# Kernel optimization log

Hardware: AMD Instinct MI355X
Metric: run time of the kernel (lower is better)

Reference implementation:

```python
import jax, jax.numpy as jnp
import numpy as np

NUM_HEADS = 16
THETA = 10000.0


def _apply_rope(x, pos):
    # x: [b, h, t, d_k], pos: [t] int
    d = x.shape[-1]
    inv_freq = THETA ** (-jnp.arange(0, d, 2, dtype=jnp.float32) / d)  # [d/2]
    ang = pos.astype(jnp.float32)[:, None] * inv_freq                  # [t, d/2]
    cos, sin = jnp.cos(ang), jnp.sin(ang)
    x1, x2 = x[..., ::2], x[..., 1::2]
    r1 = x1 * cos - x2 * sin
    r2 = x1 * sin + x2 * cos
    return jnp.stack([r1, r2], axis=-1).reshape(x.shape)


def setup_inputs() -> dict:
    key = jax.random.key(0)
    k1, k2, k3 = jax.random.split(key, 3)
    b, t, dm = 4, 2048, 2048
    in_features = jax.random.normal(k1, (b, t, dm), dtype=jnp.float32)
    token_positions = jnp.arange(t, dtype=jnp.int64)
    W_qkv = jax.random.normal(k2, (3 * dm, dm), dtype=jnp.float32) * 0.02
    W_o = jax.random.normal(k3, (dm, dm), dtype=jnp.float32) * 0.02
    return {"in_features": in_features, "token_positions": token_positions,
            "W_qkv": W_qkv, "W_o": W_o}


def reference(in_features, token_positions, W_qkv, W_o):
    b, t, dm = in_features.shape
    h = NUM_HEADS
    dk = dm // h
    # fused QKV projection (Linear: y = x W^T)
    qkv = in_features @ W_qkv.T                       # [b, t, 3*dm]
    q, k, v = jnp.split(qkv, 3, axis=-1)
    def to_heads(x):
        return x.reshape(b, t, h, dk).transpose(0, 2, 1, 3)  # [b, h, t, dk]
    q, k, v = to_heads(q), to_heads(k), to_heads(v)
    q = _apply_rope(q, token_positions)
    k = _apply_rope(k, token_positions)
    # causal SDPA
    scale = 1.0 / np.sqrt(dk).astype(np.float32)
    scores = jnp.einsum('bhqd,bhkd->bhqk', q, k) * scale
    causal = jnp.tril(jnp.ones((t, t), dtype=bool))
    scores = jnp.where(causal, scores, jnp.finfo(scores.dtype).min)
    attn = jax.nn.softmax(scores, axis=-1)
    out = jnp.einsum('bhqk,bhkd->bhqd', attn, v)      # [b, h, t, dk]
    out = out.transpose(0, 2, 1, 3).reshape(b, t, dm)
    return out @ W_o.T
```

## Files before the change

kernel.cpp:

```cpp
#include <hip/hip_runtime.h>

typedef unsigned short u16;
typedef __attribute__((ext_vector_type(8))) short s8v;
typedef __attribute__((ext_vector_type(8))) __bf16 bf8;
typedef __attribute__((ext_vector_type(4))) float f4v;

#define GLB(p) ((const __attribute__((address_space(1))) void*)(p))
#define LDS(p) ((__attribute__((address_space(3))) void*)(p))

static __device__ __forceinline__ float b2f(u16 u) {
    union { unsigned int i; float f; } v; v.i = ((unsigned int)u) << 16; return v.f;
}
static __device__ __forceinline__ u16 f2b(float f) {
    union { float f; unsigned int i; } v; v.f = f;
    v.i += 0x7fffu + ((v.i >> 16) & 1u);
    return (u16)(v.i >> 16);
}

__global__ __launch_bounds__(256) void k_conv(const float* __restrict__ X,
                                              const float* __restrict__ Wq,
                                              const float* __restrict__ Wo,
                                              u16* __restrict__ Xb,
                                              u16* __restrict__ Wqb,
                                              u16* __restrict__ Wob) {
    int i = blockIdx.x * 256 + threadIdx.x;
    const float* in; u16* out; int off;
    if (i < 4194304)      { in = X;  out = Xb;  off = i; }
    else if (i < 7340032) { in = Wq; out = Wqb; off = i - 4194304; }
    else                  { in = Wo; out = Wob; off = i - 7340032; }
    float4 v = ((const float4*)in)[off];
    union { u16 u[4]; unsigned long long ll; } o;
    o.u[0] = f2b(v.x); o.u[1] = f2b(v.y); o.u[2] = f2b(v.z); o.u[3] = f2b(v.w);
    ((unsigned long long*)out)[off] = o.ll;
}

template<int MODE>
__global__ __launch_bounds__(512, 2) void k_gemm_bt(
    const u16* __restrict__ A, const u16* __restrict__ B,
    int K, int N, int gx,
    u16* __restrict__ Qb, u16* __restrict__ Kb, u16* __restrict__ Vt,
    float* __restrict__ Cf, const int* __restrict__ pos)
{
    extern __shared__ __align__(16) u16 Ls[];

    const int t    = threadIdx.x;
    const int lane = t & 63;
    const int wid  = t >> 6;
    const int wm = wid >> 2, wn = wid & 3;
    const int la = lane & 15, lb = lane >> 4;

    const int bid = (int)blockIdx.x;
    const int id2 = (bid & 7) * ((int)gridDim.x >> 3) + (bid >> 3);
    const int bx = id2 % gx, by = id2 / gx;
    const long arow0 = (long)by * 256;
    const long brow0 = (long)bx * 256;

    const int sr = t >> 2;
    const int sg = (t & 3) ^ (sr & 3);
    const u16* Asrc = A + (arow0 + sr) * (long)K + sg * 8;
    const u16* Bsrc = B + (brow0 + sr) * (long)K + sg * 8;
    const long K128 = 128 * (long)K;
    u16* ldst = Ls + t * 8;

#define STG(q_, kt_) do {                                                          \
        const long ko_ = (long)(kt_) * 32;                                         \
        u16* d_ = ldst + (q_) * 16384;                                             \
        __builtin_amdgcn_global_load_lds(GLB(Asrc + ko_),         LDS(d_),         16, 0, 0); \
        __builtin_amdgcn_global_load_lds(GLB(Asrc + K128 + ko_),  LDS(d_ + 4096),  16, 0, 0); \
        __builtin_amdgcn_global_load_lds(GLB(Bsrc + ko_),         LDS(d_ + 8192),  16, 0, 0); \
        __builtin_amdgcn_global_load_lds(GLB(Bsrc + K128 + ko_),  LDS(d_ + 12288), 16, 0, 0); \
    } while (0)
#define RD(off) (*(const bf8*)(Ls + (off)))

    f4v acc[8][4];
#pragma unroll
    for (int m = 0; m < 8; m++)
#pragma unroll
        for (int n = 0; n < 4; n++) acc[m][n] = (f4v){0.f, 0.f, 0.f, 0.f};

    const int gA = (lb ^ (la & 3)) * 8;
    const int aBase = wm * 4096 + la * 32 + gA;
    const int bBase = 8192 + (wn >> 1) * 4096 + ((wn & 1) * 64 + la) * 32 + gA;

    const int NKT = K >> 5;
    STG(0, 0); STG(1, 1);
    asm volatile("s_waitcnt vmcnt(4)" ::: "memory");
    __builtin_amdgcn_s_barrier();

    for (int X = 0; X < NKT; ++X) {
        const int D = (X % 3) * 16384;
        int S = X + 2; if (S > NKT - 1) S = NKT - 1;
        STG((X + 2) % 3, S);

        bf8 aF[8], bF[4];
#pragma unroll
        for (int mi = 0; mi < 8; mi++) aF[mi] = RD(D + aBase + mi * 512);
#pragma unroll
        for (int ni = 0; ni < 4; ni++) bF[ni] = RD(D + bBase + ni * 512);

        __builtin_amdgcn_s_setprio(1);
#pragma unroll
        for (int mi = 0; mi < 8; mi++)
#pragma unroll
            for (int ni = 0; ni < 4; ni++)
                acc[mi][ni] = __builtin_amdgcn_mfma_f32_16x16x32_bf16(aF[mi], bF[ni], acc[mi][ni], 0, 0, 0);
        __builtin_amdgcn_s_setprio(0);

        asm volatile("s_waitcnt vmcnt(4)" ::: "memory");
        __builtin_amdgcn_s_barrier();
    }
    asm volatile("s_waitcnt vmcnt(0)" ::: "memory");
#undef STG
#undef RD

    if (MODE == 1) {
#pragma unroll
        for (int mi = 0; mi < 8; mi++)
#pragma unroll
            for (int ni = 0; ni < 4; ni++) {
                const long grow0 = arow0 + wm * 128 + mi * 16 + lb * 4;
                const int  gcol  = (int)brow0 + wn * 64 + ni * 16 + la;
#pragma unroll
                for (int i = 0; i < 4; i++)
                    Cf[(grow0 + i) * (long)N + gcol] = acc[mi][ni][i];
            }
        return;
    }

    __syncthreads();
    const int part = (int)(brow0 >> 11);
    const int colp = (int)brow0 & 2047;
    const int h0   = colp >> 7;
    const int bidx = (int)(arow0 >> 11);
    const int t0   = (int)arow0 & 2047;

    if (part == 2) {
#pragma unroll
        for (int mi = 0; mi < 8; mi++)
#pragma unroll
            for (int ni = 0; ni < 4; ni++) {
                const int tlb = wm * 128 + mi * 16 + lb * 4;
                const int dl  = wn * 64 + ni * 16 + la;
#pragma unroll
                for (int i2 = 0; i2 < 2; i2++) {
                    unsigned int pk = (unsigned int)f2b(acc[mi][ni][i2 * 2])
                                    | ((unsigned int)f2b(acc[mi][ni][i2 * 2 + 1]) << 16);
                    *(unsigned int*)(Ls + dl * 264 + tlb + i2 * 2) = pk;
                }
            }
        __syncthreads();
#pragma unroll
        for (int j = 0; j < 16; j++) {
            const int dl = j * 16 + wid * 2 + (lane >> 5);
            const int c  = lane & 31;
            bf8 v = *(const bf8*)(Ls + dl * 264 + c * 8);
            const long bh = (long)(bidx * 16 + h0 + (dl >> 7));
            *(bf8*)(Vt + (bh << 18) + ((long)(dl & 127) << 11) + t0 + c * 8) = v;
        }
    } else {
        u16* dst = (part == 0) ? Qb : Kb;
#pragma unroll
        for (int mi = 0; mi < 8; mi++)
#pragma unroll
            for (int ni = 0; ni < 4; ni++) {
                const int tlb = wm * 128 + mi * 16 + lb * 4;
                const int dl  = wn * 64 + ni * 16 + la;
#pragma unroll
                for (int i = 0; i < 4; i++)
                    Ls[(tlb + i) * 264 + dl] = f2b(acc[mi][ni][i]);
            }
        __syncthreads();
        const int c = t & 15;
        float invf[4];
#pragma unroll
        for (int p2 = 0; p2 < 4; p2++)
            invf[p2] = exp2f((float)(c * 4 + p2) * -0.20762050593046014f);
#pragma unroll
        for (int j = 0; j < 16; j++) {
            const int R  = j * 32 + (t >> 4);
            const int tl = R >> 1, hh = R & 1;
            s8v v = *(const s8v*)(Ls + tl * 264 + hh * 128 + c * 8);
            const float pf = (float)pos[t0 + tl];
            union { u16 u[8]; s8v v; } ov;
#pragma unroll
            for (int p2 = 0; p2 < 4; p2++) {
                float x1 = b2f((u16)v[2 * p2]);
                float x2 = b2f((u16)v[2 * p2 + 1]);
                float sn, cs;
                __sincosf(pf * invf[p2], &sn, &cs);
                ov.u[2 * p2]     = f2b(x1 * cs - x2 * sn);
                ov.u[2 * p2 + 1] = f2b(x1 * sn + x2 * cs);
            }
            const long bh = (long)(bidx * 16 + h0 + hh);
            *(s8v*)(dst + ((bh << 11) + t0 + tl) * 128 + c * 8) = ov.v;
        }
    }
}

__global__ __launch_bounds__(512) void k_attn(const u16* __restrict__ Qb,
                                              const u16* __restrict__ Kb,
                                              const u16* __restrict__ Vt,
                                              u16* __restrict__ Ob)
{
    __shared__ __align__(16) u16 Ks[2][32 * 128];
    __shared__ __align__(16) u16 Vs[2][64 * 64];
    __shared__ __align__(16) u16 Pl[8][32 * 32];

    const int tid  = threadIdx.x;
    const int lane = tid & 63;
    const int w    = tid >> 6;
    const int la = lane & 15, lb = lane >> 4;
    const int qg = 7 - ((int)blockIdx.x >> 6);
    const int bh = blockIdx.x & 63;
    const long base = (long)bh << 18;
    const int qt = qg * 8 + w;
    const int q0 = qt * 32;
    const int tiles_w = qt + 1;
    const int NT = qg * 8 + 8;
    const float scale = 0.08838834764831845f;

    bf8 qf[2][4];
#pragma unroll
    for (int m = 0; m < 2; m++)
#pragma unroll
        for (int kb = 0; kb < 4; kb++)
            qf[m][kb] = *(const bf8*)(Qb + base + (long)(q0 + m * 16 + la) * 128 + kb * 32 + lb * 8);

    f4v o[2][8];
#pragma unroll
    for (int m = 0; m < 2; m++)
#pragma unroll
        for (int n = 0; n < 8; n++) o[m][n] = (f4v){0.f, 0.f, 0.f, 0.f};
    float lst[2][4];
#pragma unroll
    for (int m = 0; m < 2; m++)
#pragma unroll
        for (int i = 0; i < 4; i++) lst[m][i] = 0.f;

    char* Pb = (char*)(Pl[w]);

    const int ko = tid * 16;
    const int kr = ko >> 8, kc = (ko & 255) ^ ((kr & 7) << 4);
    const int vo = tid * 16;
    const int vR = vo >> 7, vc = (vo & 127) ^ ((vR & 7) << 4);
    const int vd = 2 * vR + (vc >> 6), vt = (vc & 63) >> 1;

#define STAGE(buf, jt_) do {                                                        \
        const int kv0_ = (jt_) * 32;                                               \
        __builtin_amdgcn_global_load_lds(                                          \
            GLB(Kb + base + (long)(kv0_ + kr) * 128 + (kc >> 1)),                  \
            LDS((u16*)Ks[buf] + tid * 8), 16, 0, 0);                               \
        __builtin_amdgcn_global_load_lds(                                          \
            GLB(Vt + base + ((long)vd << 11) + kv0_ + vt),                         \
            LDS((u16*)Vs[buf] + tid * 8), 16, 0, 0);                               \
    } while (0)

    STAGE(0, 0);

    for (int jt = 0; jt < NT; ++jt) {
        const int buf = jt & 1;
        __syncthreads();
        if (jt + 1 < NT) STAGE(buf ^ 1, jt + 1);

        if (jt < tiles_w) {
            const char* KsB = (const char*)Ks[buf];
            const char* VsB = (const char*)Vs[buf];

            f4v s[2][2];
            s[0][0] = s[0][1] = s[1][0] = s[1][1] = (f4v){0.f, 0.f, 0.f, 0.f};
#pragma unroll
            for (int n = 0; n < 2; n++) {
                const int row = n * 16 + la;
#pragma unroll
                for (int kb = 0; kb < 4; kb++) {
                    bf8 kf = *(const bf8*)(KsB + row * 256 + ((kb * 64 + lb * 16) ^ ((row & 7) << 4)));
                    s[0][n] = __builtin_amdgcn_mfma_f32_16x16x32_bf16(qf[0][kb], kf, s[0][n], 0, 0, 0);
                    s[1][n] = __builtin_amdgcn_mfma_f32_16x16x32_bf16(qf[1][kb], kf, s[1][n], 0, 0, 0);
                }
            }

            bf8 vf[8];
#pragma unroll
            for (int nO = 0; nO < 8; nO++) {
                const int R = nO * 8 + (la >> 1);
                vf[nO] = *(const bf8*)(VsB + R * 128 + (((la & 1) * 64 + lb * 16) ^ ((R & 7) << 4)));
            }

            const bool diag = (jt == qt);
            float p[2][2][4];
#pragma unroll
            for (int m = 0; m < 2; m++)
#pragma unroll
                for (int n = 0; n < 2; n++)
#pragma unroll
                    for (int i = 0; i < 4; i++) {
                        float v = __expf(fmaf(s[m][n][i], scale, -8.0f));
                        if (diag && (n * 16 + la) > (m * 16 + lb * 4 + i)) v = 0.f;
                        p[m][n][i] = v;
                        lst[m][i] += v;
                    }

#pragma unroll
            for (int m = 0; m < 2; m++)
#pragma unroll
                for (int n = 0; n < 2; n++)
#pragma unroll
                    for (int i = 0; i < 4; i++) {
                        const int row = m * 16 + lb * 4 + i;
                        const int colb = (n * 16 + la) * 2;
                        *(u16*)(Pb + row * 64 + (colb ^ ((row & 3) << 4))) = f2b(p[m][n][i]);
                    }
            bf8 pa[2];
#pragma unroll
            for (int am = 0; am < 2; am++) {
                const int row = am * 16 + la;
                pa[am] = *(const bf8*)(Pb + row * 64 + ((lb * 16) ^ ((row & 3) << 4)));
            }
#pragma unroll
            for (int nO = 0; nO < 8; nO++) {
                o[0][nO] = __builtin_amdgcn_mfma_f32_16x16x32_bf16(pa[0], vf[nO], o[0][nO], 0, 0, 0);
                o[1][nO] = __builtin_amdgcn_mfma_f32_16x16x32_bf16(pa[1], vf[nO], o[1][nO], 0, 0, 0);
            }
        }
        __syncthreads();
    }
#undef STAGE

    float linv[2][4];
#pragma unroll
    for (int m = 0; m < 2; m++)
#pragma unroll
        for (int i = 0; i < 4; i++) {
            float l = lst[m][i];
            l += __shfl_xor(l, 1);
            l += __shfl_xor(l, 2);
            l += __shfl_xor(l, 4);
            l += __shfl_xor(l, 8);
            linv[m][i] = 1.0f / l;
        }

    const int b = bh >> 4, h = bh & 15;
#pragma unroll
    for (int m = 0; m < 2; m++)
#pragma unroll
        for (int nO = 0; nO < 8; nO++)
#pragma unroll
            for (int i = 0; i < 4; i++) {
                const int row = q0 + m * 16 + lb * 4 + i;
                const int d = nO * 16 + la;
                Ob[((long)(b * 2048 + row) << 11) + h * 128 + d] = f2b(o[m][nO][i] * linv[m][i]);
            }
}

extern "C" void kernel_launch(void* const* d_in, const int* in_sizes, int n_in,
                              void* d_out, int out_size, void* d_ws, size_t ws_size,
                              hipStream_t stream)
{
    const float* X    = (const float*)d_in[0];
    const int*   pos  = (const int*)d_in[1];
    const float* Wqkv = (const float*)d_in[2];
    const float* Wo   = (const float*)d_in[3];
    float* out = (float*)d_out;

    char* ws = (char*)d_ws;
    u16* Xb    = (u16*)(ws + 0);
    u16* Wqkvb = (u16*)(ws + 33554432);
    u16* Wob   = (u16*)(ws + 58720256);
    u16* Qb    = (u16*)(ws + 67108864);
    u16* Kb    = (u16*)(ws + 100663296);
    u16* Vt    = (u16*)(ws + 134217728);
    u16* Ob    = (u16*)(ws + 167772160);

    k_conv<<<32768, 256, 0, stream>>>(X, Wqkv, Wo, Xb, Wqkvb, Wob);
    k_gemm_bt<0><<<768, 512, 135168, stream>>>(Xb, Wqkvb, 2048, 6144, 24, Qb, Kb, Vt, nullptr, pos);
    k_attn<<<512, 512, 0, stream>>>(Qb, Kb, Vt, Ob);
    k_gemm_bt<1><<<256, 512, 98304, stream>>>(Ob, Wob, 2048, 2048, 8, nullptr, nullptr, nullptr, out, nullptr);
}
```

Baseline: 455.0 us.

## Shrink GEMM LDS footprint with double buffering and half-tile epilogue; narrow output GEMM tile

The GEMM switches from a triple-buffered LDS pipeline to double buffering with a new 8-way XOR swizzled layout. The QKV epilogue now stages one 128-row half of the tile at a time, so shared memory per block drops by half. The output projection uses 256x128 tiles and twice as many blocks, giving better CU coverage on the 2048x2048 result. The aim is higher occupancy and better load balance, at the cost of shallower prefetch and a full vmcnt(0) wait plus barrier every k-step.

Result: faster. 423.0 us (-7.0%).

```diff
diff --git a/kernel.cpp b/kernel.cpp
--- a/kernel.cpp
+++ b/kernel.cpp
@@ -41,6 +41,9 @@
     u16* __restrict__ Qb, u16* __restrict__ Kb, u16* __restrict__ Vt,
     float* __restrict__ Cf, const int* __restrict__ pos)
 {
+    constexpr int BN   = MODE ? 128 : 256;
+    constexpr int NB   = MODE ? 2 : 4;
+    constexpr int BUFS = MODE ? 12288 : 16384;
     extern __shared__ __align__(16) u16 Ls[];
 
     const int t    = threadIdx.x;
@@ -53,63 +56,79 @@
     const int id2 = (bid & 7) * ((int)gridDim.x >> 3) + (bid >> 3);
     const int bx = id2 % gx, by = id2 / gx;
     const long arow0 = (long)by * 256;
-    const long brow0 = (long)bx * 256;
-
-    const int sr = t >> 2;
-    const int sg = (t & 3) ^ (sr & 3);
-    const u16* Asrc = A + (arow0 + sr) * (long)K + sg * 8;
-    const u16* Bsrc = B + (brow0 + sr) * (long)K + sg * 8;
-    const long K128 = 128 * (long)K;
-    u16* ldst = Ls + t * 8;
-
-#define STG(q_, kt_) do {                                                          \
-        const long ko_ = (long)(kt_) * 32;                                         \
-        u16* d_ = ldst + (q_) * 16384;                                             \
-        __builtin_amdgcn_global_load_lds(GLB(Asrc + ko_),         LDS(d_),         16, 0, 0); \
-        __builtin_amdgcn_global_load_lds(GLB(Asrc + K128 + ko_),  LDS(d_ + 4096),  16, 0, 0); \
-        __builtin_amdgcn_global_load_lds(GLB(Bsrc + ko_),         LDS(d_ + 8192),  16, 0, 0); \
-        __builtin_amdgcn_global_load_lds(GLB(Bsrc + K128 + ko_),  LDS(d_ + 12288), 16, 0, 0); \
+    const long brow0 = (long)bx * BN;
+
+    const int r0 = t >> 3, sl = t & 7;
+    const int sA0 = sl ^ (r0 & 7);
+    const int sA1 = sl ^ ((r0 + 64) & 7);
+    const long RA0 = r0 + 128 * (sA0 >> 2);
+    const long RA1 = 64 + r0 + 128 * (sA1 >> 2);
+    const u16* As0 = A + (arow0 + RA0) * (long)K + (sA0 & 3) * 8;
+    const u16* As1 = A + (arow0 + RA1) * (long)K + (sA1 & 3) * 8;
+    const u16 *Bsrc0, *Bsrc1;
+    if (MODE == 0) {
+        Bsrc0 = B + (brow0 + RA0) * (long)K + (sA0 & 3) * 8;
+        Bsrc1 = B + (brow0 + RA1) * (long)K + (sA1 & 3) * 8;
+    } else {
+        const long RB0 = r0 + 64 * (sA0 >> 2);
+        Bsrc0 = B + (brow0 + RB0) * (long)K + (sA0 & 3) * 8;
+        Bsrc1 = nullptr;
+    }
+
+#define STG(q_, kt_) do {                                                        \
+        const long ko_ = (long)(kt_) * 32;                                       \
+        u16* d_ = Ls + (q_) * BUFS + t * 8;                                      \
+        __builtin_amdgcn_global_load_lds(GLB(As0 + ko_),   LDS(d_),         16, 0, 0); \
+        __builtin_amdgcn_global_load_lds(GLB(As1 + ko_),   LDS(d_ + 4096),  16, 0, 0); \
+        __builtin_amdgcn_global_load_lds(GLB(Bsrc0 + ko_), LDS(d_ + 8192),  16, 0, 0); \
+        if (MODE == 0)                                                           \
+            __builtin_amdgcn_global_load_lds(GLB(Bsrc1 + ko_), LDS(d_ + 12288), 16, 0, 0); \
     } while (0)
 #define RD(off) (*(const bf8*)(Ls + (off)))
 
-    f4v acc[8][4];
+    f4v acc[8][NB];
 #pragma unroll
     for (int m = 0; m < 8; m++)
 #pragma unroll
-        for (int n = 0; n < 4; n++) acc[m][n] = (f4v){0.f, 0.f, 0.f, 0.f};
-
-    const int gA = (lb ^ (la & 3)) * 8;
-    const int aBase = wm * 4096 + la * 32 + gA;
-    const int bBase = 8192 + (wn >> 1) * 4096 + ((wn & 1) * 64 + la) * 32 + gA;
+        for (int n = 0; n < NB; n++) acc[m][n] = (f4v){0.f, 0.f, 0.f, 0.f};
+
+    const int aOff = la * 64 + ((lb + 4 * wm) ^ (la & 7)) * 8;
+    int bOff[NB];
+#pragma unroll
+    for (int ni = 0; ni < NB; ni++) {
+        if (MODE == 0) {
+            bOff[ni] = 8192 + (wn & 1) * 4096 + ni * 1024 + la * 64
+                     + ((lb + 4 * (wn >> 1)) ^ (la & 7)) * 8;
+        } else {
+            const int Rb = wn * 32 + ni * 16;
+            bOff[ni] = 8192 + ((Rb & 63) + la) * 64
+                     + ((lb + 4 * (Rb >> 6)) ^ (la & 7)) * 8;
+        }
+    }
 
     const int NKT = K >> 5;
-    STG(0, 0); STG(1, 1);
-    asm volatile("s_waitcnt vmcnt(4)" ::: "memory");
-    __builtin_amdgcn_s_barrier();
-
+    STG(0, 0);
     for (int X = 0; X < NKT; ++X) {
-        const int D = (X % 3) * 16384;
-        int S = X + 2; if (S > NKT - 1) S = NKT - 1;
-        STG((X + 2) % 3, S);
-
-        bf8 aF[8], bF[4];
-#pragma unroll
-        for (int mi = 0; mi < 8; mi++) aF[mi] = RD(D + aBase + mi * 512);
-#pragma unroll
-        for (int ni = 0; ni < 4; ni++) bF[ni] = RD(D + bBase + ni * 512);
+        asm volatile("s_waitcnt vmcnt(0)" ::: "memory");
+        __builtin_amdgcn_s_barrier();
+        int S = X + 1; if (S > NKT - 1) S = NKT - 1;
+        STG((X + 1) & 1, S);
+
+        const int D = (X & 1) * BUFS;
+        bf8 aF[8], bF[NB];
+#pragma unroll
+        for (int mi = 0; mi < 8; mi++) aF[mi] = RD(D + aOff + mi * 1024);
+#pragma unroll
+        for (int ni = 0; ni < NB; ni++) bF[ni] = RD(D + bOff[ni]);
 
         __builtin_amdgcn_s_setprio(1);
 #pragma unroll
         for (int mi = 0; mi < 8; mi++)
 #pragma unroll
-            for (int ni = 0; ni < 4; ni++)
+            for (int ni = 0; ni < NB; ni++)
                 acc[mi][ni] = __builtin_amdgcn_mfma_f32_16x16x32_bf16(aF[mi], bF[ni], acc[mi][ni], 0, 0, 0);
         __builtin_amdgcn_s_setprio(0);
-
-        asm volatile("s_waitcnt vmcnt(4)" ::: "memory");
-        __builtin_amdgcn_s_barrier();
-    }
-    asm volatile("s_waitcnt vmcnt(0)" ::: "memory");
+    }
 #undef STG
 #undef RD
 
@@ -117,9 +136,9 @@
 #pragma unroll
         for (int mi = 0; mi < 8; mi++)
 #pragma unroll
-            for (int ni = 0; ni < 4; ni++) {
+            for (int ni = 0; ni < NB; ni++) {
                 const long grow0 = arow0 + wm * 128 + mi * 16 + lb * 4;
-                const int  gcol  = (int)brow0 + wn * 64 + ni * 16 + la;
+                const int  gcol  = (int)brow0 + wn * 32 + ni * 16 + la;
 #pragma unroll
                 for (int i = 0; i < 4; i++)
                     Cf[(grow0 + i) * (long)N + gcol] = acc[mi][ni][i];
@@ -129,70 +148,82 @@
 
     __syncthreads();
     const int part = (int)(brow0 >> 11);
-    const int colp = (int)brow0 & 2047;
-    const int h0   = colp >> 7;
+    const int h0   = ((int)brow0 & 2047) >> 7;
     const int bidx = (int)(arow0 >> 11);
     const int t0   = (int)arow0 & 2047;
 
     if (part == 2) {
 #pragma unroll
-        for (int mi = 0; mi < 8; mi++)
-#pragma unroll
-            for (int ni = 0; ni < 4; ni++) {
-                const int tlb = wm * 128 + mi * 16 + lb * 4;
-                const int dl  = wn * 64 + ni * 16 + la;
-#pragma unroll
-                for (int i2 = 0; i2 < 2; i2++) {
-                    unsigned int pk = (unsigned int)f2b(acc[mi][ni][i2 * 2])
-                                    | ((unsigned int)f2b(acc[mi][ni][i2 * 2 + 1]) << 16);
-                    *(unsigned int*)(Ls + dl * 264 + tlb + i2 * 2) = pk;
-                }
-            }
-        __syncthreads();
-#pragma unroll
-        for (int j = 0; j < 16; j++) {
-            const int dl = j * 16 + wid * 2 + (lane >> 5);
-            const int c  = lane & 31;
-            bf8 v = *(const bf8*)(Ls + dl * 264 + c * 8);
-            const long bh = (long)(bidx * 16 + h0 + (dl >> 7));
-            *(bf8*)(Vt + (bh << 18) + ((long)(dl & 127) << 11) + t0 + c * 8) = v;
+        for (int p = 0; p < 2; p++) {
+            if (wm == p) {
+#pragma unroll
+                for (int mi = 0; mi < 8; mi++)
+#pragma unroll
+                    for (int ni = 0; ni < 4; ni++) {
+                        const int tlb = mi * 16 + lb * 4;
+                        const int dl  = wn * 64 + ni * 16 + la;
+#pragma unroll
+                        for (int i2 = 0; i2 < 2; i2++) {
+                            unsigned int pk = (unsigned int)f2b(acc[mi][ni][i2 * 2])
+                                            | ((unsigned int)f2b(acc[mi][ni][i2 * 2 + 1]) << 16);
+                            *(unsigned int*)(Ls + dl * 132 + tlb + i2 * 2) = pk;
+                        }
+                    }
+            }
+            __syncthreads();
+#pragma unroll
+            for (int j = 0; j < 8; j++) {
+                const int dl  = j * 32 + wid * 4 + (lane >> 4);
+                const int tl8 = (lane & 15) * 8;
+                bf8 v = *(const bf8*)(Ls + dl * 132 + tl8);
+                const long bh = (long)(bidx * 16 + h0 + (dl >> 7));
+                *(bf8*)(Vt + (bh << 18) + ((long)(dl & 127) << 11) + t0 + p * 128 + tl8) = v;
+            }
+            __syncthreads();
         }
     } else {
         u16* dst = (part == 0) ? Qb : Kb;
-#pragma unroll
-        for (int mi = 0; mi < 8; mi++)
-#pragma unroll
-            for (int ni = 0; ni < 4; ni++) {
-                const int tlb = wm * 128 + mi * 16 + lb * 4;
-                const int dl  = wn * 64 + ni * 16 + la;
-#pragma unroll
-                for (int i = 0; i < 4; i++)
-                    Ls[(tlb + i) * 264 + dl] = f2b(acc[mi][ni][i]);
-            }
-        __syncthreads();
         const int c = t & 15;
         float invf[4];
 #pragma unroll
         for (int p2 = 0; p2 < 4; p2++)
             invf[p2] = exp2f((float)(c * 4 + p2) * -0.20762050593046014f);
 #pragma unroll
-        for (int j = 0; j < 16; j++) {
-            const int R  = j * 32 + (t >> 4);
-            const int tl = R >> 1, hh = R & 1;
-            s8v v = *(const s8v*)(Ls + tl * 264 + hh * 128 + c * 8);
-            const float pf = (float)pos[t0 + tl];
-            union { u16 u[8]; s8v v; } ov;
-#pragma unroll
-            for (int p2 = 0; p2 < 4; p2++) {
-                float x1 = b2f((u16)v[2 * p2]);
-                float x2 = b2f((u16)v[2 * p2 + 1]);
-                float sn, cs;
-                __sincosf(pf * invf[p2], &sn, &cs);
-                ov.u[2 * p2]     = f2b(x1 * cs - x2 * sn);
-                ov.u[2 * p2 + 1] = f2b(x1 * sn + x2 * cs);
-            }
-            const long bh = (long)(bidx * 16 + h0 + hh);
-            *(s8v*)(dst + ((bh << 11) + t0 + tl) * 128 + c * 8) = ov.v;
+        for (int p = 0; p < 2; p++) {
+            if (wm == p) {
+#pragma unroll
+                for (int mi = 0; mi < 8; mi++)
+#pragma unroll
+                    for (int ni = 0; ni < 4; ni++) {
+                        const int tlb = mi * 16 + lb * 4;
+                        const int dl  = wn * 64 + ni * 16 + la;
+#pragma unroll
+                        for (int i = 0; i < 4; i++)
+                            Ls[(tlb + i) * 264 + dl] = f2b(acc[mi][ni][i]);
+                    }
+            }
+            __syncthreads();
+#pragma unroll
+            for (int j = 0; j < 8; j++) {
+                const int R  = j * 32 + (t >> 4);
+                const int tl = R >> 1, hh = R & 1;
+                s8v v = *(const s8v*)(Ls + tl * 264 + hh * 128 + c * 8);
+                const int tg = t0 + p * 128 + tl;
+                const float pf = (float)pos[tg];
+                union { u16 u[8]; s8v v; } ov;
+#pragma unroll
+                for (int p2 = 0; p2 < 4; p2++) {
+                    float x1 = b2f((u16)v[2 * p2]);
+                    float x2 = b2f((u16)v[2 * p2 + 1]);
+                    float sn, cs;
+                    __sincosf(pf * invf[p2], &sn, &cs);
+                    ov.u[2 * p2]     = f2b(x1 * cs - x2 * sn);
+                    ov.u[2 * p2 + 1] = f2b(x1 * sn + x2 * cs);
+                }
+                const long bh = (long)(bidx * 16 + h0 + hh);
+                *(s8v*)(dst + ((bh << 11) + tg) * 128 + c * 8) = ov.v;
+            }
+            __syncthreads();
         }
     }
 }
@@ -372,7 +403,7 @@
     u16* Ob    = (u16*)(ws + 167772160);
 
     k_conv<<<32768, 256, 0, stream>>>(X, Wqkv, Wo, Xb, Wqkvb, Wob);
-    k_gemm_bt<0><<<768, 512, 135168, stream>>>(Xb, Wqkvb, 2048, 6144, 24, Qb, Kb, Vt, nullptr, pos);
+    k_gemm_bt<0><<<768, 512, 67584, stream>>>(Xb, Wqkvb, 2048, 6144, 24, Qb, Kb, Vt, nullptr, pos);
     k_attn<<<512, 512, 0, stream>>>(Qb, Kb, Vt, Ob);
-    k_gemm_bt<1><<<256, 512, 98304, stream>>>(Ob, Wob, 2048, 2048, 8, nullptr, nullptr, nullptr, out, nullptr);
-}
+    k_gemm_bt<1><<<512, 512, 49152, stream>>>(Ob, Wob, 2048, 2048, 16, nullptr, nullptr, nullptr, out, nullptr);
+}
```
